# Optimization experiments

Hardware: AMD Instinct MI355X
Metric: run time of the kernel (lower is better)

Reference implementation:

```python
import jax, jax.numpy as jnp
import numpy as np


def _lstm_step(x, h, c, Wih, Whh, bih, bhh):
    # torch.nn.LSTMCell gate order: i, f, g, o
    g = x @ Wih.T + h @ Whh.T + bih + bhh
    i, f, gg, o = jnp.split(g, 4, axis=-1)
    c2 = jax.nn.sigmoid(f) * c + jax.nn.sigmoid(i) * jnp.tanh(gg)
    h2 = jax.nn.sigmoid(o) * jnp.tanh(c2)
    return h2, c2


def _run_dir(x_pad, mask, h0, c0, Wih, Whh, bih, bhh, reverse):
    # Masked scan == VariableRecurrent: rows past batch_sizes[t] keep frozen state.
    def step(carry, inp):
        h, c = carry
        x_t, m = inp
        h2, c2 = _lstm_step(x_t, h, c, Wih, Whh, bih, bhh)
        m = m[:, None]
        h = jnp.where(m, h2, h)
        c = jnp.where(m, c2, c)
        return (h, c), h
    (hT, cT), outs = jax.lax.scan(step, (h0, c0), (x_pad, mask), reverse=reverse)
    return hT, cT, outs


def setup_inputs():
    key = jax.random.key(0)
    B, T, D, CELL, L = 64, 1024, 256, 128, 2
    G = 4 * CELL  # 512
    lengths = np.array([T - 8 * b for b in range(B)])  # 1024 .. 520, descending
    batch_sizes = jnp.asarray([(lengths > t).sum() for t in range(T)], dtype=jnp.int32)
    total = int(lengths.sum())  # 49408
    ks = jax.random.split(key, 5)
    inp = jax.random.normal(ks[0], (total, D), dtype=jnp.float32)
    W_ih = jax.random.normal(ks[1], (2 * L, G, D), jnp.float32) * 0.05
    W_hh = jax.random.normal(ks[2], (2 * L, G, CELL), jnp.float32) * 0.05
    b_ih = jax.random.normal(ks[3], (2 * L, G), jnp.float32) * 0.05
    b_hh = jax.random.normal(ks[4], (2 * L, G), jnp.float32) * 0.05
    h0 = jnp.zeros((2 * L, B, CELL), jnp.float32)
    c0 = jnp.zeros((2 * L, B, CELL), jnp.float32)
    return {"input": inp, "batch_sizes": batch_sizes, "h0": h0, "c0": c0,
            "W_ih": W_ih, "W_hh": W_hh, "b_ih": b_ih, "b_hh": b_hh}


def reference(input, batch_sizes, h0, c0, W_ih, W_hh, b_ih, b_hh):
    T = batch_sizes.shape[0]
    B = h0.shape[1]
    total = input.shape[0]
    num_layers = W_ih.shape[0] // 2
    # packed <-> padded index math (static shapes; values from batch_sizes)
    offsets = jnp.concatenate([jnp.zeros((1,), batch_sizes.dtype),
                               jnp.cumsum(batch_sizes)[:-1]])  # [T]
    bidx = jnp.arange(B)
    mask = bidx[None, :] < batch_sizes[:, None]  # [T, B] valid rows per step
    gather_idx = jnp.clip(offsets[:, None] + bidx[None, :], 0, total - 1)
    x = input[gather_idx]  # padded [T, B, D]; invalid rows masked in scan
    tok = jnp.arange(total)
    t_idx = jnp.searchsorted(offsets, tok, side='right') - 1
    b_idx = tok - offsets[t_idx]
    hs, cs = [], []
    for l in range(num_layers):
        outs = []
        for d in range(2):  # layer ordering: fwd_l, rev_l (matches StackedRNN)
            k = 2 * l + d
            hT, cT, o = _run_dir(x, mask, h0[k], c0[k],
                                 W_ih[k], W_hh[k], b_ih[k], b_hh[k],
                                 reverse=(d == 1))
            hs.append(hT)
            cs.append(cT)
            outs.append(o)
        x = jnp.concatenate(outs, axis=-1)  # [T, B, hidden_size]
    h_n = jnp.stack(hs, 0)  # [total_layers, B, CELL]
    c_n = jnp.stack(cs, 0)
    packed_out = x[t_idx, b_idx]  # [total, hidden_size]
    return packed_out, h_n, c_n
```

## Files before the change

kernel.cpp:

```cpp
#include <hip/hip_runtime.h>
#include <hip/hip_fp16.h>
#include <hip/hip_bf16.h>


#define CELL 128
#define GATES 512
#define DIN 256
#define NB 64

typedef float f4_t __attribute__((ext_vector_type(4)));
typedef short bf8_t __attribute__((ext_vector_type(8)));
typedef _Float16 h2_t __attribute__((ext_vector_type(2)));

static __device__ __forceinline__ unsigned short f32_bf16(float f) {
  union { float f; unsigned int u; } v; v.f = f;
  unsigned int u = v.u;
  return (unsigned short)((u + 0x7fffu + ((u >> 16) & 1u)) >> 16);
}

__global__ void k_setup(const int* __restrict__ bs, int T,
                        int* __restrict__ offsets, int* __restrict__ lengths) {
  __shared__ int sbs[1024];
  int t = threadIdx.x;
  sbs[t] = (t < T) ? bs[t] : 0;
  __syncthreads();
  int sum = 0;
  for (int i = 0; i < t; ++i) sum += sbs[i];
  if (t < T) offsets[t] = sum;
  if (t < NB) {
    int c = 0;
    for (int i = 0; i < T; ++i) c += (sbs[i] > t) ? 1 : 0;
    lengths[t] = c;
  }
}

__global__ void k_convert(const float* __restrict__ x, unsigned short* __restrict__ xb, int nx,
                          const float* __restrict__ wih, unsigned short* __restrict__ wb, int nw,
                          const float* __restrict__ bih, const float* __restrict__ bhh,
                          float* __restrict__ bsum, int nb2) {
  int stride = gridDim.x * blockDim.x;
  int i0 = blockIdx.x * blockDim.x + threadIdx.x;
  for (int i = i0; i < nx; i += stride) xb[i] = f32_bf16(x[i]);
  for (int i = i0; i < nw; i += stride) wb[i] = f32_bf16(wih[i]);
  for (int i = i0; i < nb2; i += stride) bsum[i] = bih[i] + bhh[i];
}

__global__ __launch_bounds__(256) void k_gemm(
    const unsigned short* __restrict__ A,
    const unsigned short* __restrict__ W,
    const float* __restrict__ bsum,
    __half* __restrict__ C,
    int M, int lbase) {
  __shared__ __align__(16) unsigned short As[128 * 64];
  __shared__ __align__(16) unsigned short Bs[128 * 64];
  const int tid = threadIdx.x;
  const int lane = tid & 63;
  const int wave = tid >> 6;
  const int wm = wave >> 1, wn = wave & 1;
  const int m0 = blockIdx.x * 128;
  const int n0 = blockIdx.y * 128;

  f4_t acc[4][4];
#pragma unroll
  for (int i = 0; i < 4; ++i)
#pragma unroll
    for (int j = 0; j < 4; ++j) acc[i][j] = (f4_t){0.f, 0.f, 0.f, 0.f};

  for (int kt = 0; kt < 256; kt += 64) {
#pragma unroll
    for (int it = 0; it < 4; ++it) {
      int idx = it * 256 + tid;
      int row = idx >> 3;
      int gslot = (idx & 7) ^ (row & 7);
      int grow = m0 + row; if (grow > M - 1) grow = M - 1;
      __builtin_amdgcn_global_load_lds(
          (const __attribute__((address_space(1))) unsigned int*)(A + (size_t)grow * 256 + kt + gslot * 8),
          (__attribute__((address_space(3))) unsigned int*)(As + idx * 8), 16, 0, 0);
    }
#pragma unroll
    for (int it = 0; it < 4; ++it) {
      int idx = it * 256 + tid;
      int row = idx >> 3;
      int gslot = (idx & 7) ^ (row & 7);
      __builtin_amdgcn_global_load_lds(
          (const __attribute__((address_space(1))) unsigned int*)(W + (size_t)(lbase + n0 + row) * 256 + kt + gslot * 8),
          (__attribute__((address_space(3))) unsigned int*)(Bs + idx * 8), 16, 0, 0);
    }
    asm volatile("s_waitcnt vmcnt(0)" ::: "memory");
    __syncthreads();
#pragma unroll
    for (int kk = 0; kk < 2; ++kk) {
      bf8_t af[4], bfv[4];
#pragma unroll
      for (int i = 0; i < 4; ++i) {
        int arow = wm * 64 + i * 16 + (lane & 15);
        int aslot = (kk * 4 + (lane >> 4)) ^ (arow & 7);
        af[i] = *(const bf8_t*)(As + arow * 64 + aslot * 8);
        int brow = wn * 64 + i * 16 + (lane & 15);
        int bslot = (kk * 4 + (lane >> 4)) ^ (brow & 7);
        bfv[i] = *(const bf8_t*)(Bs + brow * 64 + bslot * 8);
      }
#pragma unroll
      for (int i = 0; i < 4; ++i)
#pragma unroll
        for (int j = 0; j < 4; ++j)
          acc[i][j] = __builtin_amdgcn_mfma_f32_16x16x32_bf16(af[i], bfv[j], acc[i][j], 0, 0, 0);
    }
    __syncthreads();
  }
#pragma unroll
  for (int i = 0; i < 4; ++i) {
#pragma unroll
    for (int j = 0; j < 4; ++j) {
      int col = n0 + wn * 64 + j * 16 + (lane & 15);
      float bv = bsum[lbase + col];
#pragma unroll
      for (int r = 0; r < 4; ++r) {
        int row = m0 + wm * 64 + i * 16 + (lane >> 4) * 4 + r;
        if (row < M) C[(size_t)row * 1024 + col] = (__half)(acc[i][j][r] + bv);
      }
    }
  }
}

#if defined(__has_builtin)
#if __has_builtin(__builtin_amdgcn_fdot2)
#define HAVE_FDOT2 1
#endif
#endif

static __device__ __forceinline__ float fdot2(h2_t a, h2_t b, float c) {
#ifdef HAVE_FDOT2
  return __builtin_amdgcn_fdot2(a, b, c, false);
#else
  return c + (float)a[0] * (float)b[0] + (float)a[1] * (float)b[1];
#endif
}
static __device__ __forceinline__ float sigm(float x) { return 1.f / (1.f + __expf(-x)); }
static __device__ __forceinline__ float tanh_(float x) { return 1.f - 2.f / (1.f + __expf(2.f * x)); }

template <int LAYER>
__global__ __launch_bounds__(512) void k_rec(
    const __half* __restrict__ gates,
    const int* __restrict__ offsets,
    const int* __restrict__ lengths,
    const float* __restrict__ h0,
    const float* __restrict__ c0,
    const float* __restrict__ Whh,
    unsigned short* __restrict__ y1,
    float* __restrict__ outp,
    float* __restrict__ hn, float* __restrict__ cn,
    int T) {
  const int b = blockIdx.x >> 1;
  const int d = blockIdx.x & 1;
  const int k = 2 * LAYER + d;
  const int tid = threadIdx.x;
  const int q = tid & 127;
  const int s = tid >> 7;
  const int L = lengths[b];

  __shared__ __align__(16) __half hbuf[CELL];
  __shared__ float4 part[512];
  __shared__ int toks[1024];

  for (int t = tid; t < T; t += 512) toks[t] = offsets[t] + b;

  h2_t wp[4][16];
  {
    const float* Wb = Whh + (size_t)k * GATES * CELL;
#pragma unroll
    for (int gi = 0; gi < 4; ++gi) {
      const float* rowp = Wb + (size_t)(gi * CELL + q) * CELL + s * 32;
#pragma unroll
      for (int j = 0; j < 16; ++j) {
        h2_t p; p[0] = (_Float16)rowp[2 * j]; p[1] = (_Float16)rowp[2 * j + 1];
        wp[gi][j] = p;
      }
    }
  }

  float hcur = 0.f, ccur = 0.f;
  if (tid < CELL) {
    hcur = h0[(size_t)k * NB * CELL + b * CELL + q];
    ccur = c0[(size_t)k * NB * CELL + b * CELL + q];
    hbuf[q] = (__half)hcur;
  }
  __syncthreads();

  __half gx0 = __half(0.f), gx1 = __half(0.f), gx2 = __half(0.f), gx3 = __half(0.f);
  int tokc = 0;
  if (tid < CELL && L > 0) {
    tokc = toks[d ? (L - 1) : 0];
    const __half* gp = gates + (size_t)tokc * 1024 + d * GATES + q;
    gx0 = gp[0]; gx1 = gp[CELL]; gx2 = gp[2 * CELL]; gx3 = gp[3 * CELL];
  }

  for (int n = 0; n < L; ++n) {
    const h2_t* hsh = (const h2_t*)hbuf;
    h2_t hp[16];
#pragma unroll
    for (int j = 0; j < 16; ++j) hp[j] = hsh[s * 16 + j];
    float a0 = 0.f, a1 = 0.f, a2 = 0.f, a3 = 0.f;
#pragma unroll
    for (int j = 0; j < 16; ++j) {
      a0 = fdot2(wp[0][j], hp[j], a0);
      a1 = fdot2(wp[1][j], hp[j], a1);
      a2 = fdot2(wp[2][j], hp[j], a2);
      a3 = fdot2(wp[3][j], hp[j], a3);
    }
    part[tid] = make_float4(a0, a1, a2, a3);
    __syncthreads();
    if (tid < CELL) {
      float4 v0 = part[q], v1 = part[q + 128], v2 = part[q + 256], v3 = part[q + 384];
      float gi = v0.x + v1.x + v2.x + v3.x + __half2float(gx0);
      float gf = v0.y + v1.y + v2.y + v3.y + __half2float(gx1);
      float gg = v0.z + v1.z + v2.z + v3.z + __half2float(gx2);
      float go = v0.w + v1.w + v2.w + v3.w + __half2float(gx3);
      int tokn = tokc;
      if (n + 1 < L) {
        tokn = toks[d ? (L - 2 - n) : (n + 1)];
        const __half* gp = gates + (size_t)tokn * 1024 + d * GATES + q;
        gx0 = gp[0]; gx1 = gp[CELL]; gx2 = gp[2 * CELL]; gx3 = gp[3 * CELL];
      }
      float fi = sigm(gi), ff = sigm(gf), fg = tanh_(gg), fo = sigm(go);
      ccur = ff * ccur + fi * fg;
      hcur = fo * tanh_(ccur);
      hbuf[q] = (__half)hcur;
      if (LAYER == 0)
        y1[(size_t)tokc * 256 + d * CELL + q] = f32_bf16(hcur);
      else
        outp[(size_t)tokc * 256 + d * CELL + q] = hcur;
      tokc = tokn;
    }
    __syncthreads();
  }
  if (tid < CELL) {
    hn[(size_t)k * NB * CELL + b * CELL + q] = hcur;
    cn[(size_t)k * NB * CELL + b * CELL + q] = ccur;
  }
}

extern "C" void kernel_launch(void* const* d_in, const int* in_sizes, int n_in,
                              void* d_out, int out_size, void* d_ws, size_t ws_size,
                              hipStream_t stream) {
  const float* x   = (const float*)d_in[0];
  const int*   bs  = (const int*)d_in[1];
  const float* h0  = (const float*)d_in[2];
  const float* c0  = (const float*)d_in[3];
  const float* wih = (const float*)d_in[4];
  const float* whh = (const float*)d_in[5];
  const float* bih = (const float*)d_in[6];
  const float* bhh = (const float*)d_in[7];
  const int TOTAL = in_sizes[0] / DIN;
  const int T = in_sizes[1];

  char* ws = (char*)d_ws;
  size_t off = 0;
  auto alloc = [&](size_t bytes) {
    void* p = ws + off;
    off = (off + bytes + 255) & ~(size_t)255;
    return p;
  };
  int* offsets        = (int*)alloc((size_t)T * 4);
  int* lengths        = (int*)alloc(NB * 4);
  float* bsum         = (float*)alloc(2048 * 4);
  unsigned short* wb  = (unsigned short*)alloc((size_t)2048 * 256 * 2);
  unsigned short* xb  = (unsigned short*)alloc((size_t)TOTAL * 256 * 2);
  unsigned short* y1  = (unsigned short*)alloc((size_t)TOTAL * 256 * 2);
  __half* gates       = (__half*)alloc((size_t)TOTAL * 1024 * 2);

  float* outp = (float*)d_out;
  float* hn = outp + (size_t)TOTAL * 256;
  float* cn = hn + 4 * NB * CELL;

  k_setup<<<1, 1024, 0, stream>>>(bs, T, offsets, lengths);
  k_convert<<<1024, 256, 0, stream>>>(x, xb, TOTAL * 256,
                                      wih, wb, 4 * GATES * DIN,
                                      bih, bhh, bsum, 2048);
  dim3 ggrid((TOTAL + 127) / 128, 8);
  k_gemm<<<ggrid, 256, 0, stream>>>(xb, wb, bsum, gates, TOTAL, 0);
  k_rec<0><<<NB * 2, 512, 0, stream>>>(gates, offsets, lengths, h0, c0, whh,
                                       y1, nullptr, hn, cn, T);
  k_gemm<<<ggrid, 256, 0, stream>>>(y1, wb, bsum, gates, TOTAL, 1024);
  k_rec<1><<<NB * 2, 512, 0, stream>>>(gates, offsets, lengths, h0, c0, whh,
                                       nullptr, outp, hn, cn, T);
}
```

Baseline: 1.745 ms.

## Reduce recurrent matvec partials with wave shuffles and double-buffer hidden state

```diff
diff --git a/kernel.cpp b/kernel.cpp
--- a/kernel.cpp
+++ b/kernel.cpp
@@ -138,6 +138,13 @@
 }
 static __device__ __forceinline__ float sigm(float x) { return 1.f / (1.f + __expf(-x)); }
 static __device__ __forceinline__ float tanh_(float x) { return 1.f - 2.f / (1.f + __expf(2.f * x)); }
+
+static __device__ __forceinline__ float red16(float v) {
+  return v + __int_as_float(__builtin_amdgcn_ds_swizzle(__float_as_int(v), 0x401F));
+}
+static __device__ __forceinline__ float red32(float v) {
+  return v + __shfl_xor(v, 32, 64);
+}
 
 template <int LAYER>
 __global__ __launch_bounds__(512) void k_rec(
@@ -155,12 +162,13 @@
   const int d = blockIdx.x & 1;
   const int k = 2 * LAYER + d;
   const int tid = threadIdx.x;
-  const int q = tid & 127;
-  const int s = tid >> 7;
+  const int lane = tid & 63;
+  const int wave = tid >> 6;
+  const int q = wave * 16 + (lane & 15);
+  const int s = lane >> 4;
   const int L = lengths[b];
 
-  __shared__ __align__(16) __half hbuf[CELL];
-  __shared__ float4 part[512];
+  __shared__ __align__(16) __half hb[2][CELL];
   __shared__ int toks[1024];
 
   for (int t = tid; t < T; t += 512) toks[t] = offsets[t] + b;
@@ -170,33 +178,40 @@
     const float* Wb = Whh + (size_t)k * GATES * CELL;
 #pragma unroll
     for (int gi = 0; gi < 4; ++gi) {
-      const float* rowp = Wb + (size_t)(gi * CELL + q) * CELL + s * 32;
+      const float2* rowp = (const float2*)(Wb + (size_t)(gi * CELL + q) * CELL + s * 32);
 #pragma unroll
       for (int j = 0; j < 16; ++j) {
-        h2_t p; p[0] = (_Float16)rowp[2 * j]; p[1] = (_Float16)rowp[2 * j + 1];
+        float2 w = rowp[j];
+        h2_t p; p[0] = (_Float16)w.x; p[1] = (_Float16)w.y;
         wp[gi][j] = p;
       }
     }
   }
 
-  float hcur = 0.f, ccur = 0.f;
-  if (tid < CELL) {
-    hcur = h0[(size_t)k * NB * CELL + b * CELL + q];
-    ccur = c0[(size_t)k * NB * CELL + b * CELL + q];
-    hbuf[q] = (__half)hcur;
-  }
+  float hcur = h0[(size_t)k * NB * CELL + b * CELL + q];
+  float ccur = c0[(size_t)k * NB * CELL + b * CELL + q];
+  if (s == 0) hb[0][q] = (__half)hcur;
   __syncthreads();
 
   __half gx0 = __half(0.f), gx1 = __half(0.f), gx2 = __half(0.f), gx3 = __half(0.f);
   int tokc = 0;
-  if (tid < CELL && L > 0) {
+  if (L > 0) {
     tokc = toks[d ? (L - 1) : 0];
     const __half* gp = gates + (size_t)tokc * 1024 + d * GATES + q;
     gx0 = gp[0]; gx1 = gp[CELL]; gx2 = gp[2 * CELL]; gx3 = gp[3 * CELL];
   }
 
+  int p = 0;
   for (int n = 0; n < L; ++n) {
-    const h2_t* hsh = (const h2_t*)hbuf;
+    int tokn = tokc;
+    if (n + 1 < L) tokn = toks[d ? (L - 2 - n) : (n + 1)];
+    __half gn0, gn1, gn2, gn3;
+    {
+      const __half* gp = gates + (size_t)tokn * 1024 + d * GATES + q;
+      gn0 = gp[0]; gn1 = gp[CELL]; gn2 = gp[2 * CELL]; gn3 = gp[3 * CELL];
+    }
+
+    const h2_t* hsh = (const h2_t*)hb[p];
     h2_t hp[16];
 #pragma unroll
     for (int j = 0; j < 16; ++j) hp[j] = hsh[s * 16 + j];
@@ -208,33 +223,32 @@
       a2 = fdot2(wp[2][j], hp[j], a2);
       a3 = fdot2(wp[3][j], hp[j], a3);
     }
-    part[tid] = make_float4(a0, a1, a2, a3);
-    __syncthreads();
-    if (tid < CELL) {
-      float4 v0 = part[q], v1 = part[q + 128], v2 = part[q + 256], v3 = part[q + 384];
-      float gi = v0.x + v1.x + v2.x + v3.x + __half2float(gx0);
-      float gf = v0.y + v1.y + v2.y + v3.y + __half2float(gx1);
-      float gg = v0.z + v1.z + v2.z + v3.z + __half2float(gx2);
-      float go = v0.w + v1.w + v2.w + v3.w + __half2float(gx3);
-      int tokn = tokc;
-      if (n + 1 < L) {
-        tokn = toks[d ? (L - 2 - n) : (n + 1)];
-        const __half* gp = gates + (size_t)tokn * 1024 + d * GATES + q;
-        gx0 = gp[0]; gx1 = gp[CELL]; gx2 = gp[2 * CELL]; gx3 = gp[3 * CELL];
-      }
-      float fi = sigm(gi), ff = sigm(gf), fg = tanh_(gg), fo = sigm(go);
-      ccur = ff * ccur + fi * fg;
-      hcur = fo * tanh_(ccur);
-      hbuf[q] = (__half)hcur;
+    a0 = red32(red16(a0));
+    a1 = red32(red16(a1));
+    a2 = red32(red16(a2));
+    a3 = red32(red16(a3));
+
+    float gi = a0 + __half2float(gx0);
+    float gf = a1 + __half2float(gx1);
+    float gg = a2 + __half2float(gx2);
+    float go = a3 + __half2float(gx3);
+    float fi = sigm(gi), ff = sigm(gf), fg = tanh_(gg), fo = sigm(go);
+    ccur = ff * ccur + fi * fg;
+    hcur = fo * tanh_(ccur);
+
+    if (s == 0) {
+      hb[p ^ 1][q] = (__half)hcur;
       if (LAYER == 0)
         y1[(size_t)tokc * 256 + d * CELL + q] = f32_bf16(hcur);
       else
         outp[(size_t)tokc * 256 + d * CELL + q] = hcur;
-      tokc = tokn;
     }
     __syncthreads();
-  }
-  if (tid < CELL) {
+    p ^= 1;
+    gx0 = gn0; gx1 = gn1; gx2 = gn2; gx3 = gn3;
+    tokc = tokn;
+  }
+  if (s == 0) {
     hn[(size_t)k * NB * CELL + b * CELL + q] = hcur;
     cn[(size_t)k * NB * CELL + b * CELL + q] = ccur;
   }
```

Result: slower. 1.946 ms (+11.6%).
